# Performance work log

Measured on AMD Instinct MI355X. Metric: run time of the kernel, lower is better.

Reference implementation:

```python
import jax, jax.numpy as jnp
import numpy as np

N_HEADS = 4
T_OUT = 24  # total T; y has T - t_in steps


def setup_inputs() -> dict:
    key = jax.random.key(0)
    k1, k2, k3, k4 = jax.random.split(key, 4)
    B, t_in, N, C, K = 2, 12, 10000, 16, 17  # K = k + 1 (self)
    x = jax.random.normal(k1, (B, t_in, N, C), dtype=jnp.float32)
    nearest_nodes = jax.random.randint(k2, (N, K), 0, N, dtype=jnp.int32)
    nearest_dists = jax.random.uniform(k3, (N, K), dtype=jnp.float32)
    shrink_w = jax.random.normal(k4, (T_OUT - t_in, t_in * N_HEADS), dtype=jnp.float32) * 0.1
    shrink_b = jnp.zeros((T_OUT - t_in,), dtype=jnp.float32)
    return {"x": x, "nearest_nodes": nearest_nodes, "nearest_dists": nearest_dists,
            "shrink_w": shrink_w, "shrink_b": shrink_b}


def reference(x, nearest_nodes, nearest_dists, shrink_w, shrink_b):
    B, t_in, N, C = x.shape
    H = N_HEADS
    # sigma = nearest_dists.max() / sigma_ratio, with sigma_ratio = 1
    sigma = jnp.max(nearest_dists)
    lam = jnp.arange(1, H + 1, dtype=x.dtype) / H  # (H,)
    # distance weights per head: (N, K, H)
    w = jnp.exp(-(nearest_dists[..., None] ** 2) * lam / (sigma ** 2))
    w = jnp.where((nearest_nodes == -1)[..., None], 0.0, w)
    w = jnp.where(w < 1e-8, 0.0, w)
    # pad node at index N; -1 neighbors map to pad (weight already zero)
    pad_x = jnp.concatenate([x, jnp.zeros_like(x[:, :, :1])], axis=2)  # (B,T,N+1,C)
    idx = jnp.where(nearest_nodes == -1, N, nearest_nodes)  # (N, K)
    g = pad_x[:, :, idx]  # (B, t_in, N, K, C) neighbor gather
    # weighted reduce over neighbor axis -> (B, t_in, N, H, C)
    agg = jnp.einsum('btnkc,nkh->btnhc', g, w)
    # (B, N, C, t_in*H)
    a = jnp.transpose(agg, (0, 2, 4, 1, 3)).reshape(B, N, C, t_in * H)
    y = a @ shrink_w.T + shrink_b  # (B, N, C, T - t_in)
    y = jnp.transpose(y, (0, 3, 1, 2))  # (B, T - t_in, N, C)
    y = jax.nn.selu(y)  # CustomActivationFunction default mode='selu'
    return jnp.concatenate([x, y], axis=1)  # (B, T, N, C)
```

## Files before the change

### kernel.cpp

```cpp
#include <hip/hip_runtime.h>
#include <hip/hip_bf16.h>
#include <math.h>

#define NB      2
#define T_IN    12
#define T_OUT_  24
#define O_OUT   12
#define NN      10000
#define CC      16
#define KK      17
#define HH      4
#define JJ      48
#define NPC     80
#define NCHUNK  125
#define PPG     3

__device__ __forceinline__ unsigned short f2bf(float f) {
    union { float f; unsigned int u; } v; v.f = f;
    unsigned int r = v.u + 0x7FFFu + ((v.u >> 16) & 1u);
    return (unsigned short)(r >> 16);
}
__device__ __forceinline__ float bf2f(unsigned int lo16) {
    union { unsigned int u; float f; } v; v.u = lo16 << 16;
    return v.f;
}

__global__ void sigma_reduce_kernel(const float* __restrict__ d, int n,
                                    unsigned int* __restrict__ out) {
    float m = 0.0f;
    for (int i = blockIdx.x * blockDim.x + threadIdx.x; i < n;
         i += gridDim.x * blockDim.x)
        m = fmaxf(m, d[i]);
    #pragma unroll
    for (int off = 32; off > 0; off >>= 1)
        m = fmaxf(m, __shfl_down(m, off, 64));
    __shared__ float sm[8];
    int lane = threadIdx.x & 63, wid = threadIdx.x >> 6;
    if (lane == 0) sm[wid] = m;
    __syncthreads();
    if (threadIdx.x == 0) {
        float mm = sm[0];
        int nw = (blockDim.x + 63) >> 6;
        for (int w = 1; w < nw; ++w) mm = fmaxf(mm, sm[w]);
        atomicMax(out, __float_as_uint(mm));
    }
}

__global__ __launch_bounds__(256) void weights_kernel(
    const int* __restrict__ nodes, const float* __restrict__ dists,
    const unsigned int* __restrict__ sigma_bits,
    int* __restrict__ idxf, uint2* __restrict__ wpk)
{
    int i = blockIdx.x * 256 + threadIdx.x;
    if (i >= NN * KK) return;
    const float sigma  = __uint_as_float(*sigma_bits);
    const float inv_s2 = 1.0f / (sigma * sigma);
    const int   nd = nodes[i];
    const float d  = dists[i];
    const float q  = d * d * inv_s2;
    float w[HH];
    #pragma unroll
    for (int h = 0; h < HH; ++h) {
        float ww = expf(-q * (float)(h + 1) * 0.25f);
        if (nd == -1 || ww < 1e-8f) ww = 0.0f;
        w[h] = ww;
    }
    idxf[i] = ((nd < 0) ? 0 : nd) * (CC * 4);
    uint2 p;
    p.x = (unsigned)f2bf(w[0]) | ((unsigned)f2bf(w[1]) << 16);
    p.y = (unsigned)f2bf(w[2]) | ((unsigned)f2bf(w[3]) << 16);
    wpk[i] = p;
}

__global__ __launch_bounds__(256) void aggregate_kernel(
    const float* __restrict__ x,
    const int*   __restrict__ idxf,
    const uint2* __restrict__ wpk,
    float* __restrict__ out,
    unsigned short* __restrict__ agg)
{
    const int g     = blockIdx.x & 7;
    const int chunk = blockIdx.x >> 3;
    const int n0    = chunk * NPC;
    const int tid   = threadIdx.x;

    __shared__ int   lds_idx[NPC * KK];
    __shared__ float lds_w[NPC * KK][HH];

    const int rbase = n0 * KK;
    for (int j = tid; j < NPC * KK; j += 256) {
        lds_idx[j] = idxf[rbase + j];
        const uint2 wp = wpk[rbase + j];
        lds_w[j][0] = bf2f(wp.x & 0xffffu);
        lds_w[j][1] = bf2f(wp.x >> 16);
        lds_w[j][2] = bf2f(wp.y & 0xffffu);
        lds_w[j][3] = bf2f(wp.y >> 16);
    }
    __syncthreads();

    int plane[PPG], bb[PPG], tt[PPG];
    const char* xb[PPG];
    #pragma unroll
    for (int p = 0; p < PPG; ++p) {
        plane[p] = g + 8 * p;
        bb[p] = plane[p] / T_IN;
        tt[p] = plane[p] % T_IN;
        xb[p] = (const char*)(x + (long)plane[p] * NN * CC);
    }

    const int c  = tid & 15;
    const int nl = tid >> 4;
    const int cb = c * 4;

    for (int it = 0; it < NPC / 16; ++it) {
        const int n_local = nl + 16 * it;
        const int n  = n0 + n_local;
        const int rb = n_local * KK;

        float a0[PPG], a1[PPG], a2[PPG], a3[PPG];
        #pragma unroll
        for (int p = 0; p < PPG; ++p) { a0[p]=0.f; a1[p]=0.f; a2[p]=0.f; a3[p]=0.f; }

        #pragma unroll
        for (int k = 0; k < KK; ++k) {
            const int   off = lds_idx[rb + k] + cb;
            const float w0 = lds_w[rb + k][0];
            const float w1 = lds_w[rb + k][1];
            const float w2 = lds_w[rb + k][2];
            const float w3 = lds_w[rb + k][3];
            float gv[PPG];
            #pragma unroll
            for (int p = 0; p < PPG; ++p)
                gv[p] = *(const float*)(xb[p] + off);
            #pragma unroll
            for (int p = 0; p < PPG; ++p) {
                a0[p] += gv[p] * w0;
                a1[p] += gv[p] * w1;
                a2[p] += gv[p] * w2;
                a3[p] += gv[p] * w3;
            }
        }

        #pragma unroll
        for (int p = 0; p < PPG; ++p) {
            uint2 pk;
            pk.x = (unsigned)f2bf(a0[p]) | ((unsigned)f2bf(a1[p]) << 16);
            pk.y = (unsigned)f2bf(a2[p]) | ((unsigned)f2bf(a3[p]) << 16);
            ((uint2*)agg)[(((n * NB + bb[p]) * T_IN + tt[p]) * CC) + c] = pk;
        }
    }

    #pragma unroll
    for (int p = 0; p < PPG; ++p) {
        const float4* src = (const float4*)(x + (long)plane[p] * NN * CC + n0 * CC);
        float4* dst = (float4*)(out + (long)(bb[p] * T_OUT_ + tt[p]) * NN * CC + n0 * CC);
        for (int i = tid; i < NPC * CC / 4; i += 256)
            dst[i] = src[i];
    }
}

__global__ __launch_bounds__(384) void shrink_kernel(
    const unsigned short* __restrict__ agg,
    const float* __restrict__ Wm, const float* __restrict__ bias,
    float* __restrict__ out)
{
    const int n   = blockIdx.x;
    const int tid = threadIdx.x;

    __shared__ float a_s[NB * T_IN * CC * HH];
    __shared__ float W_s[O_OUT * JJ];
    __shared__ float b_s[O_OUT];

    const uint2 v = ((const uint2*)(agg + (long)n * (NB * T_IN * CC * HH)))[tid];
    a_s[4 * tid + 0] = bf2f(v.x & 0xffffu);
    a_s[4 * tid + 1] = bf2f(v.x >> 16);
    a_s[4 * tid + 2] = bf2f(v.y & 0xffffu);
    a_s[4 * tid + 3] = bf2f(v.y >> 16);
    for (int i = tid; i < O_OUT * JJ; i += 384) W_s[i] = Wm[i];
    if (tid < O_OUT) b_s[tid] = bias[tid];
    __syncthreads();

    const int c2   = tid & 15;
    const int rest = tid >> 4;
    const int o    = rest % O_OUT;
    const int b2   = rest / O_OUT;

    float y = b_s[o];
    #pragma unroll
    for (int t = 0; t < T_IN; ++t) {
        const int ab = ((b2 * T_IN + t) * CC + c2) * HH;
        const int wb = o * JJ + t * HH;
        #pragma unroll
        for (int h = 0; h < HH; ++h)
            y += a_s[ab + h] * W_s[wb + h];
    }

    const float kScale = 1.0507009873554805f;
    const float kAlpha = 1.6732632423543772f;
    y = (y > 0.0f) ? kScale * y : kScale * kAlpha * expm1f(y);

    out[((long)(b2 * T_OUT_ + T_IN + o) * NN + n) * CC + c2] = y;
}

extern "C" void kernel_launch(void* const* d_in, const int* in_sizes, int n_in,
                              void* d_out, int out_size, void* d_ws, size_t ws_size,
                              hipStream_t stream) {
    const float* x     = (const float*)d_in[0];
    const int*   nodes = (const int*)  d_in[1];
    const float* dists = (const float*)d_in[2];
    const float* Wm    = (const float*)d_in[3];
    const float* bias  = (const float*)d_in[4];
    float* out = (float*)d_out;

    char* ws = (char*)d_ws;
    unsigned int*   sigma_bits = (unsigned int*)ws;
    int*            idxf = (int*)(ws + 256);
    uint2*          wpk  = (uint2*)(ws + 256 + 680000);
    unsigned short* agg  = (unsigned short*)(ws + 256 + 680000 + 1360000);

    hipMemsetAsync(d_ws, 0, 4, stream);

    const int nd = in_sizes[2];
    sigma_reduce_kernel<<<256, 256, 0, stream>>>(dists, nd, sigma_bits);
    weights_kernel<<<(NN * KK + 255) / 256, 256, 0, stream>>>(
        nodes, dists, sigma_bits, idxf, wpk);
    aggregate_kernel<<<8 * NCHUNK, 256, 0, stream>>>(x, idxf, wpk, out, agg);
    shrink_kernel<<<NN, 384, 0, stream>>>(agg, Wm, bias, out);
}
```

Baseline: 126.7 us.

## Fuse weight computation into aggregation, single-block sigma, multi-node shrink blocks

The separate weights kernel is removed and each aggregate block now computes its neighbor weights from nodes and dists straight into LDS. The four head weights come from one exp and its powers, and the weights stay in fp32 rather than going through bf16. Sigma is reduced by a single 1024-thread block with vectorized loads, which drops the memset and the atomic. The shrink kernel now handles four nodes per block and reads agg directly from global memory instead of staging it in LDS. Together these cut kernel launches and workspace traffic, but each of the 8 plane-groups now recomputes the exp weights for its chunk, and the single-block sigma pass is serial.

Result: slower. 139.7 us (+10.3%).

```diff
diff --git a/kernel.cpp b/kernel.cpp
--- a/kernel.cpp
+++ b/kernel.cpp
@@ -14,6 +14,7 @@
 #define NPC     80
 #define NCHUNK  125
 #define PPG     3
+#define NPS     4
 
 __device__ __forceinline__ unsigned short f2bf(float f) {
     union { float f; unsigned int u; } v; v.f = f;
@@ -25,57 +26,36 @@
     return v.f;
 }
 
-__global__ void sigma_reduce_kernel(const float* __restrict__ d, int n,
-                                    unsigned int* __restrict__ out) {
+__global__ __launch_bounds__(1024) void sigma_single_kernel(
+    const float* __restrict__ d, int n, unsigned int* __restrict__ out) {
     float m = 0.0f;
-    for (int i = blockIdx.x * blockDim.x + threadIdx.x; i < n;
-         i += gridDim.x * blockDim.x)
-        m = fmaxf(m, d[i]);
+    const int nv4 = n >> 2;
+    const float4* d4 = (const float4*)d;
+    for (int i = threadIdx.x; i < nv4; i += 1024) {
+        float4 v = d4[i];
+        m = fmaxf(fmaxf(m, fmaxf(v.x, v.y)), fmaxf(v.z, v.w));
+    }
+    for (int i = (nv4 << 2) + threadIdx.x; i < n; i += 1024) m = fmaxf(m, d[i]);
     #pragma unroll
     for (int off = 32; off > 0; off >>= 1)
         m = fmaxf(m, __shfl_down(m, off, 64));
-    __shared__ float sm[8];
+    __shared__ float sm[16];
     int lane = threadIdx.x & 63, wid = threadIdx.x >> 6;
     if (lane == 0) sm[wid] = m;
     __syncthreads();
     if (threadIdx.x == 0) {
         float mm = sm[0];
-        int nw = (blockDim.x + 63) >> 6;
-        for (int w = 1; w < nw; ++w) mm = fmaxf(mm, sm[w]);
-        atomicMax(out, __float_as_uint(mm));
-    }
-}
-
-__global__ __launch_bounds__(256) void weights_kernel(
-    const int* __restrict__ nodes, const float* __restrict__ dists,
-    const unsigned int* __restrict__ sigma_bits,
-    int* __restrict__ idxf, uint2* __restrict__ wpk)
-{
-    int i = blockIdx.x * 256 + threadIdx.x;
-    if (i >= NN * KK) return;
-    const float sigma  = __uint_as_float(*sigma_bits);
-    const float inv_s2 = 1.0f / (sigma * sigma);
-    const int   nd = nodes[i];
-    const float d  = dists[i];
-    const float q  = d * d * inv_s2;
-    float w[HH];
-    #pragma unroll
-    for (int h = 0; h < HH; ++h) {
-        float ww = expf(-q * (float)(h + 1) * 0.25f);
-        if (nd == -1 || ww < 1e-8f) ww = 0.0f;
-        w[h] = ww;
-    }
-    idxf[i] = ((nd < 0) ? 0 : nd) * (CC * 4);
-    uint2 p;
-    p.x = (unsigned)f2bf(w[0]) | ((unsigned)f2bf(w[1]) << 16);
-    p.y = (unsigned)f2bf(w[2]) | ((unsigned)f2bf(w[3]) << 16);
-    wpk[i] = p;
+        #pragma unroll
+        for (int w = 1; w < 16; ++w) mm = fmaxf(mm, sm[w]);
+        *out = __float_as_uint(mm);
+    }
 }
 
 __global__ __launch_bounds__(256) void aggregate_kernel(
     const float* __restrict__ x,
-    const int*   __restrict__ idxf,
-    const uint2* __restrict__ wpk,
+    const int*   __restrict__ nodes,
+    const float* __restrict__ dists,
+    const unsigned int* __restrict__ sigma_bits,
     float* __restrict__ out,
     unsigned short* __restrict__ agg)
 {
@@ -87,14 +67,22 @@
     __shared__ int   lds_idx[NPC * KK];
     __shared__ float lds_w[NPC * KK][HH];
 
+    const float sigma  = __uint_as_float(*sigma_bits);
+    const float inv_s2 = 1.0f / (sigma * sigma);
     const int rbase = n0 * KK;
     for (int j = tid; j < NPC * KK; j += 256) {
-        lds_idx[j] = idxf[rbase + j];
-        const uint2 wp = wpk[rbase + j];
-        lds_w[j][0] = bf2f(wp.x & 0xffffu);
-        lds_w[j][1] = bf2f(wp.x >> 16);
-        lds_w[j][2] = bf2f(wp.y & 0xffffu);
-        lds_w[j][3] = bf2f(wp.y >> 16);
+        const int   nd = nodes[rbase + j];
+        const float dd = dists[rbase + j];
+        const float q  = dd * dd * inv_s2;
+        const float e1 = expf(-q * 0.25f);
+        float w0 = e1, w1 = e1 * e1, w2 = w1 * e1, w3 = w1 * w1;
+        if (nd == -1) { w0 = w1 = w2 = w3 = 0.f; }
+        if (w0 < 1e-8f) w0 = 0.f;
+        if (w1 < 1e-8f) w1 = 0.f;
+        if (w2 < 1e-8f) w2 = 0.f;
+        if (w3 < 1e-8f) w3 = 0.f;
+        lds_idx[j]   = ((nd < 0) ? 0 : nd) * (CC * 4);
+        lds_w[j][0] = w0; lds_w[j][1] = w1; lds_w[j][2] = w2; lds_w[j][3] = w3;
     }
     __syncthreads();
 
@@ -164,42 +152,42 @@
     const float* __restrict__ Wm, const float* __restrict__ bias,
     float* __restrict__ out)
 {
-    const int n   = blockIdx.x;
     const int tid = threadIdx.x;
 
-    __shared__ float a_s[NB * T_IN * CC * HH];
     __shared__ float W_s[O_OUT * JJ];
     __shared__ float b_s[O_OUT];
 
-    const uint2 v = ((const uint2*)(agg + (long)n * (NB * T_IN * CC * HH)))[tid];
-    a_s[4 * tid + 0] = bf2f(v.x & 0xffffu);
-    a_s[4 * tid + 1] = bf2f(v.x >> 16);
-    a_s[4 * tid + 2] = bf2f(v.y & 0xffffu);
-    a_s[4 * tid + 3] = bf2f(v.y >> 16);
     for (int i = tid; i < O_OUT * JJ; i += 384) W_s[i] = Wm[i];
     if (tid < O_OUT) b_s[tid] = bias[tid];
     __syncthreads();
 
-    const int c2   = tid & 15;
+    const int c    = tid & 15;
     const int rest = tid >> 4;
     const int o    = rest % O_OUT;
-    const int b2   = rest / O_OUT;
-
-    float y = b_s[o];
-    #pragma unroll
-    for (int t = 0; t < T_IN; ++t) {
-        const int ab = ((b2 * T_IN + t) * CC + c2) * HH;
-        const int wb = o * JJ + t * HH;
-        #pragma unroll
-        for (int h = 0; h < HH; ++h)
-            y += a_s[ab + h] * W_s[wb + h];
-    }
+    const int b    = rest / O_OUT;
 
     const float kScale = 1.0507009873554805f;
     const float kAlpha = 1.6732632423543772f;
-    y = (y > 0.0f) ? kScale * y : kScale * kAlpha * expm1f(y);
-
-    out[((long)(b2 * T_OUT_ + T_IN + o) * NN + n) * CC + c2] = y;
+
+    #pragma unroll
+    for (int u = 0; u < NPS; ++u) {
+        const int n = blockIdx.x * NPS + u;
+        const uint2* ap = (const uint2*)agg + ((long)(n * NB + b) * T_IN) * CC + c;
+
+        float y = b_s[o];
+        #pragma unroll
+        for (int t = 0; t < T_IN; ++t) {
+            const uint2 v = ap[t * CC];
+            const int wb = o * JJ + t * HH;
+            y += bf2f(v.x & 0xffffu) * W_s[wb + 0];
+            y += bf2f(v.x >> 16)     * W_s[wb + 1];
+            y += bf2f(v.y & 0xffffu) * W_s[wb + 2];
+            y += bf2f(v.y >> 16)     * W_s[wb + 3];
+        }
+
+        y = (y > 0.0f) ? kScale * y : kScale * kAlpha * expm1f(y);
+        out[((long)(b * T_OUT_ + T_IN + o) * NN + n) * CC + c] = y;
+    }
 }
 
 extern "C" void kernel_launch(void* const* d_in, const int* in_sizes, int n_in,
@@ -214,16 +202,11 @@
 
     char* ws = (char*)d_ws;
     unsigned int*   sigma_bits = (unsigned int*)ws;
-    int*            idxf = (int*)(ws + 256);
-    uint2*          wpk  = (uint2*)(ws + 256 + 680000);
-    unsigned short* agg  = (unsigned short*)(ws + 256 + 680000 + 1360000);
-
-    hipMemsetAsync(d_ws, 0, 4, stream);
+    unsigned short* agg        = (unsigned short*)(ws + 256);
 
     const int nd = in_sizes[2];
-    sigma_reduce_kernel<<<256, 256, 0, stream>>>(dists, nd, sigma_bits);
-    weights_kernel<<<(NN * KK + 255) / 256, 256, 0, stream>>>(
-        nodes, dists, sigma_bits, idxf, wpk);
-    aggregate_kernel<<<8 * NCHUNK, 256, 0, stream>>>(x, idxf, wpk, out, agg);
-    shrink_kernel<<<NN, 384, 0, stream>>>(agg, Wm, bias, out);
-}
+    sigma_single_kernel<<<1, 1024, 0, stream>>>(dists, nd, sigma_bits);
+    aggregate_kernel<<<8 * NCHUNK, 256, 0, stream>>>(x, nodes, dists,
+                                                     sigma_bits, out, agg);
+    shrink_kernel<<<NN / NPS, 384, 0, stream>>>(agg, Wm, bias, out);
+}
```
